# Kernel optimization log

Hardware: AMD Instinct MI355X
Metric: run time of the kernel (lower is better)

The kernel has to match this reference:

```python
import jax, jax.numpy as jnp
import numpy as np

B, N, D = 8192, 49, 3
D3 = 42  # embed_dim // 3
E = 128
K = 3    # min(3, N-1) nearest neighbors for local density


def setup_inputs() -> dict:
    key = jax.random.key(0)
    ks = jax.random.split(key, 8)
    points = jax.random.normal(ks[0], (B, N, D), jnp.float32)
    return {
        "points": points,
        "W_dist": jax.random.normal(ks[1], (1, D3), jnp.float32) * 1.0,
        "b_dist": jnp.zeros((D3,), jnp.float32),
        "emb": jax.random.normal(ks[2], (50, D3), jnp.float32) * 0.02,
        "W_den": jax.random.normal(ks[3], (1, D3), jnp.float32) * 1.0,
        "b_den": jnp.zeros((D3,), jnp.float32),
        "W_out": jax.random.normal(ks[4], (3 * D3, E), jnp.float32) * (1.0 / np.sqrt(3 * D3)),
        "b_out": jnp.zeros((E,), jnp.float32),
    }


def _local_density(points):
    # Batched cdist with diagonal masked to +inf, then mean of K smallest dists.
    sq = jnp.sum(points * points, axis=-1)                      # [B,N]
    d2 = sq[:, :, None] + sq[:, None, :] \
         - 2.0 * jnp.einsum('bnd,bmd->bnm', points, points)      # [B,N,N]
    d2 = jnp.maximum(d2, 0.0)
    eye = jnp.eye(points.shape[1], dtype=bool)
    d2 = jnp.where(eye, jnp.inf, d2)
    dists = jnp.sqrt(d2)
    nearest = -jax.lax.top_k(-dists, K)[0]                      # [B,N,K] smallest
    return jnp.mean(nearest, axis=-1, keepdims=True)            # [B,N,1]


def reference(points, W_dist, b_dist, emb, W_den, b_den, W_out, b_out):
    b, n, _ = points.shape
    centroid = jnp.mean(points, axis=1, keepdims=True)          # [B,1,3]
    rel = points - centroid
    centroid_dist = jnp.linalg.norm(rel, axis=-1, keepdims=True)  # [B,N,1]
    dist_f = centroid_dist @ W_dist + b_dist                    # [B,N,D3]
    # n_valid == N (no mask), a constant index into the count embedding
    count_f = jnp.broadcast_to(emb[n][None, None, :], (b, n, emb.shape[1]))
    density = _local_density(points)                            # [B,N,1]
    den_f = density @ W_den + b_den                             # [B,N,D3]
    features = jnp.concatenate([dist_f, count_f, den_f], axis=-1)  # [B,N,3*D3]
    return features @ W_out + b_out                             # [B,N,E]
```

## Files before the change

kernel.cpp:

```cpp
#include <hip/hip_runtime.h>
#include <math.h>

#define N_   49
#define D3_  42
#define E_   128

__global__ void precompute_uvc(const float* __restrict__ W_dist,
                               const float* __restrict__ b_dist,
                               const float* __restrict__ emb,
                               const float* __restrict__ W_den,
                               const float* __restrict__ b_den,
                               const float* __restrict__ W_out,
                               const float* __restrict__ b_out,
                               float* __restrict__ uvc) {
    int e = threadIdx.x;
    if (e >= E_) return;
    const float* embN = emb + N_ * D3_;
    float u = 0.f, v = 0.f, c = b_out[e];
    for (int j = 0; j < D3_; ++j) {
        float w0 = W_out[j * E_ + e];
        float w1 = W_out[(D3_ + j) * E_ + e];
        float w2 = W_out[(2 * D3_ + j) * E_ + e];
        u = fmaf(W_dist[j], w0, u);
        v = fmaf(W_den[j], w2, v);
        c = fmaf(b_dist[j], w0, c);
        c = fmaf(embN[j], w1, c);
        c = fmaf(b_den[j], w2, c);
    }
    uvc[e]          = u;
    uvc[E_ + e]     = v;
    uvc[2 * E_ + e] = c;
}

__global__ __launch_bounds__(256) void rank2_feature_kernel(
        const float* __restrict__ points,
        const float* __restrict__ uvc,
        float* __restrict__ out) {
    __shared__ float pts[N_ * 3];
    __shared__ __align__(16) float sU[E_];
    __shared__ __align__(16) float sV[E_];
    __shared__ __align__(16) float sC[E_];
    __shared__ float cent[3];
    __shared__ float cd[N_];
    __shared__ float den[N_];

    const int tid = threadIdx.x;
    const long long b = blockIdx.x;
    const float* pb = points + b * (N_ * 3);

    if (tid < N_ * 3) pts[tid] = pb[tid];
    if (tid < E_) {
        sU[tid] = uvc[tid];
        sV[tid] = uvc[E_ + tid];
        sC[tid] = uvc[2 * E_ + tid];
    }
    __syncthreads();

    if (tid < 3) {
        float s = 0.f;
        for (int i = 0; i < N_; ++i) s += pts[3 * i + tid];
        cent[tid] = s * (1.0f / N_);
    }
    __syncthreads();

    if (tid < N_) {
        const int n = tid;
        const float px = pts[3 * n], py = pts[3 * n + 1], pz = pts[3 * n + 2];

        {
            float dx = px - cent[0], dy = py - cent[1], dz = pz - cent[2];
            cd[n] = sqrtf(dx * dx + dy * dy + dz * dz);
        }

        float s0 = INFINITY, s1 = INFINITY, s2 = INFINITY;
        for (int m = 0; m < N_; ++m) {
            float dx = px - pts[3 * m];
            float dy = py - pts[3 * m + 1];
            float dz = pz - pts[3 * m + 2];
            float d2 = dx * dx + dy * dy + dz * dz;
            if (m != n) {
                if (d2 < s0)      { s2 = s1; s1 = s0; s0 = d2; }
                else if (d2 < s1) { s2 = s1; s1 = d2; }
                else if (d2 < s2) { s2 = d2; }
            }
        }
        den[n] = (sqrtf(s0) + sqrtf(s1) + sqrtf(s2)) * (1.0f / 3.0f);
    }
    __syncthreads();

    const float4* u4 = (const float4*)sU;
    const float4* v4 = (const float4*)sV;
    const float4* c4 = (const float4*)sC;
    float* outb = out + b * (long long)(N_ * E_);
    for (int i = tid; i < N_ * (E_ / 4); i += 256) {
        int n = i >> 5;
        int q = i & 31;
        float a = cd[n];
        float d = den[n];
        float4 u = u4[q], v = v4[q], c = c4[q];
        float4 r;
        r.x = fmaf(a, u.x, fmaf(d, v.x, c.x));
        r.y = fmaf(a, u.y, fmaf(d, v.y, c.y));
        r.z = fmaf(a, u.z, fmaf(d, v.z, c.z));
        r.w = fmaf(a, u.w, fmaf(d, v.w, c.w));
        ((float4*)(outb + n * E_))[q] = r;
    }
}

extern "C" void kernel_launch(void* const* d_in, const int* in_sizes, int n_in,
                              void* d_out, int out_size, void* d_ws, size_t ws_size,
                              hipStream_t stream) {
    const float* points = (const float*)d_in[0];
    const float* W_dist = (const float*)d_in[1];
    const float* b_dist = (const float*)d_in[2];
    const float* emb    = (const float*)d_in[3];
    const float* W_den  = (const float*)d_in[4];
    const float* b_den  = (const float*)d_in[5];
    const float* W_out  = (const float*)d_in[6];
    const float* b_out  = (const float*)d_in[7];
    float* out = (float*)d_out;
    float* uvc = (float*)d_ws;

    int B = in_sizes[0] / (N_ * 3);

    precompute_uvc<<<1, 128, 0, stream>>>(W_dist, b_dist, emb, W_den, b_den,
                                          W_out, b_out, uvc);
    rank2_feature_kernel<<<B, 256, 0, stream>>>(points, uvc, out);
}
```

Measured before the change: 245.4 us.

## Split density computation and output write into separate kernels

Splits the fused per-batch kernel in two. The first kernel uses 64 threads per batch to compute centroid distance and local density, folding the centroid sum into the neighbor loop, and stores them as float2 in workspace. The second is a grid-stride kernel that streams the rank-2 output rows using u/v/c held in registers. This aims to stop most threads idling during the O(N^2) density phase and to make the write phase a pure bandwidth stream. The cost is an extra launch and a workspace round-trip.

```diff
diff --git a/kernel.cpp b/kernel.cpp
--- a/kernel.cpp
+++ b/kernel.cpp
@@ -4,6 +4,7 @@
 #define N_   49
 #define D3_  42
 #define E_   128
+
 
 __global__ void precompute_uvc(const float* __restrict__ W_dist,
                                const float* __restrict__ b_dist,
@@ -32,78 +33,60 @@
     uvc[2 * E_ + e] = c;
 }
 
-__global__ __launch_bounds__(256) void rank2_feature_kernel(
+__global__ __launch_bounds__(64) void compute_cdden(
         const float* __restrict__ points,
-        const float* __restrict__ uvc,
-        float* __restrict__ out) {
+        float2* __restrict__ cdden) {
     __shared__ float pts[N_ * 3];
-    __shared__ __align__(16) float sU[E_];
-    __shared__ __align__(16) float sV[E_];
-    __shared__ __align__(16) float sC[E_];
-    __shared__ float cent[3];
-    __shared__ float cd[N_];
-    __shared__ float den[N_];
-
     const int tid = threadIdx.x;
     const long long b = blockIdx.x;
     const float* pb = points + b * (N_ * 3);
 
-    if (tid < N_ * 3) pts[tid] = pb[tid];
-    if (tid < E_) {
-        sU[tid] = uvc[tid];
-        sV[tid] = uvc[E_ + tid];
-        sC[tid] = uvc[2 * E_ + tid];
-    }
-    __syncthreads();
-
-    if (tid < 3) {
-        float s = 0.f;
-        for (int i = 0; i < N_; ++i) s += pts[3 * i + tid];
-        cent[tid] = s * (1.0f / N_);
-    }
+    for (int i = tid; i < N_ * 3; i += 64) pts[i] = pb[i];
     __syncthreads();
 
     if (tid < N_) {
-        const int n = tid;
-        const float px = pts[3 * n], py = pts[3 * n + 1], pz = pts[3 * n + 2];
-
-        {
-            float dx = px - cent[0], dy = py - cent[1], dz = pz - cent[2];
-            cd[n] = sqrtf(dx * dx + dy * dy + dz * dz);
-        }
-
+        const float px = pts[3 * tid], py = pts[3 * tid + 1], pz = pts[3 * tid + 2];
+        float sx = 0.f, sy = 0.f, sz = 0.f;
         float s0 = INFINITY, s1 = INFINITY, s2 = INFINITY;
         for (int m = 0; m < N_; ++m) {
-            float dx = px - pts[3 * m];
-            float dy = py - pts[3 * m + 1];
-            float dz = pz - pts[3 * m + 2];
-            float d2 = dx * dx + dy * dy + dz * dz;
-            if (m != n) {
+            float qx = pts[3 * m], qy = pts[3 * m + 1], qz = pts[3 * m + 2];
+            sx += qx; sy += qy; sz += qz;
+            float dx = px - qx, dy = py - qy, dz = pz - qz;
+            float d2 = fmaf(dx, dx, fmaf(dy, dy, dz * dz));
+            if (m != tid) {
                 if (d2 < s0)      { s2 = s1; s1 = s0; s0 = d2; }
                 else if (d2 < s1) { s2 = s1; s1 = d2; }
                 else if (d2 < s2) { s2 = d2; }
             }
         }
-        den[n] = (sqrtf(s0) + sqrtf(s1) + sqrtf(s2)) * (1.0f / 3.0f);
+        const float inv = 1.0f / (float)N_;
+        float cx = sx * inv, cy = sy * inv, cz = sz * inv;
+        float dx = px - cx, dy = py - cy, dz = pz - cz;
+        float cd  = sqrtf(fmaf(dx, dx, fmaf(dy, dy, dz * dz)));
+        float den = (sqrtf(s0) + sqrtf(s1) + sqrtf(s2)) * (1.0f / 3.0f);
+        cdden[b * N_ + tid] = make_float2(cd, den);
     }
-    __syncthreads();
+}
 
-    const float4* u4 = (const float4*)sU;
-    const float4* v4 = (const float4*)sV;
-    const float4* c4 = (const float4*)sC;
-    float* outb = out + b * (long long)(N_ * E_);
-    for (int i = tid; i < N_ * (E_ / 4); i += 256) {
-        int n = i >> 5;
-        int q = i & 31;
-        float a = cd[n];
-        float d = den[n];
-        float4 u = u4[q], v = v4[q], c = c4[q];
-        float4 r;
-        r.x = fmaf(a, u.x, fmaf(d, v.x, c.x));
-        r.y = fmaf(a, u.y, fmaf(d, v.y, c.y));
-        r.z = fmaf(a, u.z, fmaf(d, v.z, c.z));
-        r.w = fmaf(a, u.w, fmaf(d, v.w, c.w));
-        ((float4*)(outb + n * E_))[q] = r;
+__global__ __launch_bounds__(256) void rank2_write(
+        const float2* __restrict__ cdden,
+        const float4* __restrict__ uvc4,
+        float4* __restrict__ out4,
+        int total_rows) {
+    const int q   = threadIdx.x & 31;
+    const int sub = threadIdx.x >> 5;
+    const float4 u = uvc4[q];
+    const float4 v = uvc4[32 + q];
+    const float4 c = uvc4[64 + q];
+    const long long stride = (long long)gridDim.x * 8;
+    for (long long r = (long long)blockIdx.x * 8 + sub; r < total_rows; r += stride) {
+        float2 ad = cdden[r];
+        float4 w;
+        w.x = fmaf(ad.x, u.x, fmaf(ad.y, v.x, c.x));
+        w.y = fmaf(ad.x, u.y, fmaf(ad.y, v.y, c.y));
+        w.z = fmaf(ad.x, u.z, fmaf(ad.y, v.z, c.z));
+        w.w = fmaf(ad.x, u.w, fmaf(ad.y, v.w, c.w));
+        out4[r * 32 + q] = w;
     }
 }
 
@@ -118,12 +101,16 @@
     const float* b_den  = (const float*)d_in[5];
     const float* W_out  = (const float*)d_in[6];
     const float* b_out  = (const float*)d_in[7];
-    float* out = (float*)d_out;
-    float* uvc = (float*)d_ws;
 
-    int B = in_sizes[0] / (N_ * 3);
+    float*  uvc   = (float*)d_ws;
+    float2* cdden = (float2*)((char*)d_ws + 1536);
+
+    const int B = in_sizes[0] / (N_ * 3);
+    const int total_rows = B * N_;
 
     precompute_uvc<<<1, 128, 0, stream>>>(W_dist, b_dist, emb, W_den, b_den,
                                           W_out, b_out, uvc);
-    rank2_feature_kernel<<<B, 256, 0, stream>>>(points, uvc, out);
+    compute_cdden<<<B, 64, 0, stream>>>(points, cdden);
+    rank2_write<<<4096, 256, 0, stream>>>(cdden, (const float4*)uvc,
+                                          (float4*)d_out, total_rows);
 }
```

Measured after the change: 238.5 us. -2.8%, faster.
